# Kernel optimization log

Measured on AMD Instinct MI355X. Metric: run time of the kernel, lower is better.

## Reference

```python
import jax, jax.numpy as jnp
import numpy as np

EPS = 1e-12
SIMILARITY = 'l2'


def setup_inputs() -> dict:
    key = jax.random.key(0)
    k1, k2, k3, k4 = jax.random.split(key, 4)
    N, M, D = 8192, 8192, 256
    x = jax.random.normal(k1, (N, D), dtype=jnp.float32)
    x_n = jax.random.normal(k2, (M, D), dtype=jnp.float32)
    W = jax.random.normal(k3, (D, 2), dtype=jnp.float32) / np.sqrt(D)
    b = jax.random.normal(k4, (2,), dtype=jnp.float32)
    return {"x": x, "x_n": x_n, "W": W, "b": b}


def _sim_matrix(x, x_n, similarity):
    if similarity == 'l2':
        x2 = jnp.sum(x * x, axis=1, keepdims=True)          # [N,1]
        xn2 = jnp.sum(x_n * x_n, axis=1, keepdims=True).T    # [1,M]
        d2 = jnp.maximum(x2 + xn2 - 2.0 * (x @ x_n.T), 0.0)
        return -jnp.sqrt(d2)
    elif similarity == 'l1':
        return -jnp.sum(jnp.abs(x[:, None, :] - x_n[None, :, :]), axis=-1)
    elif similarity == 'dot':
        return (x @ x_n.T) / x.shape[1]
    elif similarity == 'cos':
        xn_ = x / jnp.linalg.norm(x, axis=1, keepdims=True)
        xnn = x_n / jnp.linalg.norm(x_n, axis=1, keepdims=True)
        return xn_ @ xnn.T
    raise ValueError(similarity)


def reference(x, x_n, W, b) -> jnp.ndarray:
    # soft-KNN params from a small linear head
    params = jax.nn.sigmoid(x @ W + b)                      # [N,2]
    k = jnp.clip(params[:, 0:1], EPS, 1.0 - EPS)            # [N,1]
    t = jnp.clip(params[:, 1:2], EPS, 1.0 - EPS)            # [N,1]

    sim = _sim_matrix(x, x_n, SIMILARITY)                   # [N,M]
    sim_min = jnp.min(sim, axis=1, keepdims=True)
    sim_max = jnp.max(sim, axis=1, keepdims=True)
    sim = (sim - sim_min) / (sim_max - sim_min)             # row min-max normalize
    sim = jnp.maximum(sim, EPS)

    shift = t / (1.0 - t) * (k - sim) * jnp.log(sim / k)
    return sim + jnp.where(sim <= k, shift, 0.0)
```

## Files before the change

### kernel.cpp

```cpp
#include <hip/hip_runtime.h>
#include <hip/hip_bf16.h>
#include <cstdint>

#define N_ROWS 8192
#define M_ROWS 8192
#define DDIM   256
#define EPSF   1e-12f

typedef unsigned short u16;
typedef __attribute__((ext_vector_type(8))) short short8;
typedef __attribute__((ext_vector_type(4))) float floatx4;

__device__ inline void split_bf16(float v, u16& h, u16& lo) {
    __hip_bfloat16 hb = __float2bfloat16(v);
    float hf = __bfloat162float(hb);
    __hip_bfloat16 lb = __float2bfloat16(v - hf);
    h  = __builtin_bit_cast(u16, hb);
    lo = __builtin_bit_cast(u16, lb);
}

__global__ __launch_bounds__(256) void prep_x(
    const float* __restrict__ x, const float* __restrict__ W, const float* __restrict__ b,
    u16* __restrict__ xhi, u16* __restrict__ xlo,
    float* __restrict__ x2, float* __restrict__ karr, float* __restrict__ Carr,
    float* __restrict__ logkarr)
{
    const int l = threadIdx.x & 63;
    const int w = threadIdx.x >> 6;
    const int row = blockIdx.x * 4 + w;

    const float4 xv = *(const float4*)(x + (size_t)row * DDIM + l * 4);
    const float4 wa = *(const float4*)(W + l * 8);
    const float4 wb = *(const float4*)(W + l * 8 + 4);

    float s2 = xv.x * xv.x + xv.y * xv.y + xv.z * xv.z + xv.w * xv.w;
    float s0 = xv.x * wa.x + xv.y * wa.z + xv.z * wb.x + xv.w * wb.z;
    float s1 = xv.x * wa.y + xv.y * wa.w + xv.z * wb.y + xv.w * wb.w;

    u16 h0, l0, h1, l1, h2, l2, h3, l3;
    split_bf16(xv.x, h0, l0); split_bf16(xv.y, h1, l1);
    split_bf16(xv.z, h2, l2); split_bf16(xv.w, h3, l3);
    *(ushort4*)(xhi + (size_t)row * DDIM + l * 4) = make_ushort4(h0, h1, h2, h3);
    *(ushort4*)(xlo + (size_t)row * DDIM + l * 4) = make_ushort4(l0, l1, l2, l3);

    #pragma unroll
    for (int off = 32; off; off >>= 1) {
        s2 += __shfl_xor(s2, off);
        s0 += __shfl_xor(s0, off);
        s1 += __shfl_xor(s1, off);
    }
    if (l == 0) {
        float a0 = s0 + b[0];
        float a1 = s1 + b[1];
        float k = 1.0f / (1.0f + __expf(-a0));
        float t = 1.0f / (1.0f + __expf(-a1));
        k = fminf(fmaxf(k, EPSF), 1.0f - EPSF);
        t = fminf(fmaxf(t, EPSF), 1.0f - EPSF);
        x2[row] = s2;
        karr[row] = k;
        Carr[row] = t / (1.0f - t);
        logkarr[row] = logf(k);
    }
}

__global__ __launch_bounds__(256) void prep_xn(
    const float* __restrict__ xn,
    u16* __restrict__ xnhi, u16* __restrict__ xnlo, float* __restrict__ xn2)
{
    const int l = threadIdx.x & 63;
    const int w = threadIdx.x >> 6;
    const int row = blockIdx.x * 4 + w;

    const float4 xv = *(const float4*)(xn + (size_t)row * DDIM + l * 4);
    float s2 = xv.x * xv.x + xv.y * xv.y + xv.z * xv.z + xv.w * xv.w;

    u16 h0, l0, h1, l1, h2, l2, h3, l3;
    split_bf16(xv.x, h0, l0); split_bf16(xv.y, h1, l1);
    split_bf16(xv.z, h2, l2); split_bf16(xv.w, h3, l3);
    *(ushort4*)(xnhi + (size_t)row * DDIM + l * 4) = make_ushort4(h0, h1, h2, h3);
    *(ushort4*)(xnlo + (size_t)row * DDIM + l * 4) = make_ushort4(l0, l1, l2, l3);

    #pragma unroll
    for (int off = 32; off; off >>= 1) s2 += __shfl_xor(s2, off);
    if (l == 0) xn2[row] = s2;
}

__global__ __launch_bounds__(256) void gemm_s(
    const u16* __restrict__ xhi, const u16* __restrict__ xlo,
    const u16* __restrict__ xnhi, const u16* __restrict__ xnlo,
    const float* __restrict__ x2, const float* __restrict__ xn2,
    float* __restrict__ out)
{
    __shared__ u16 lds[16384];

    const int l  = threadIdx.x & 63;
    const int w  = threadIdx.x >> 6;
    const int wm = w >> 1;
    const int wn = w & 1;
    const int bRow = blockIdx.y;
    const int bCol = blockIdx.x;

    floatx4 acc[4][4];
    #pragma unroll
    for (int mi = 0; mi < 4; ++mi)
        #pragma unroll
        for (int ni = 0; ni < 4; ++ni)
            acc[mi][ni] = (floatx4){0.f, 0.f, 0.f, 0.f};

    const u16* bases[4] = {xhi, xlo, xnhi, xnlo};
    const int lrow = l & 15;
    const int lk8  = (l >> 4) * 8;

    for (int kk = 0; kk < DDIM / 32; ++kk) {
        const int ks = kk * 32;
        #pragma unroll
        for (int p = 0; p < 8; ++p) {
            const int id    = w * 8 + p;
            const int panel = id >> 3;
            const int tile  = id & 7;
            const int grow  = (panel < 2 ? bRow : bCol) * 128 + tile * 16 + lrow;
            const u16* src  = bases[panel] + (size_t)grow * DDIM + ks + lk8;
            u16* dst = &lds[panel * 4096 + tile * 512];
            __builtin_amdgcn_global_load_lds(
                (const __attribute__((address_space(1))) void*)src,
                (__attribute__((address_space(3))) void*)dst,
                16, 0, 0);
        }
        __syncthreads();

        short8 ah[4], al[4], bh[4], bl[4];
        #pragma unroll
        for (int i = 0; i < 4; ++i) {
            ah[i] = *(const short8*)&lds[0     + (wm * 4 + i) * 512 + l * 8];
            al[i] = *(const short8*)&lds[4096  + (wm * 4 + i) * 512 + l * 8];
            bh[i] = *(const short8*)&lds[8192  + (wn * 4 + i) * 512 + l * 8];
            bl[i] = *(const short8*)&lds[12288 + (wn * 4 + i) * 512 + l * 8];
        }
        #pragma unroll
        for (int mi = 0; mi < 4; ++mi)
            #pragma unroll
            for (int ni = 0; ni < 4; ++ni) {
                acc[mi][ni] = __builtin_amdgcn_mfma_f32_16x16x32_bf16(ah[mi], bh[ni], acc[mi][ni], 0, 0, 0);
                acc[mi][ni] = __builtin_amdgcn_mfma_f32_16x16x32_bf16(ah[mi], bl[ni], acc[mi][ni], 0, 0, 0);
                acc[mi][ni] = __builtin_amdgcn_mfma_f32_16x16x32_bf16(al[mi], bh[ni], acc[mi][ni], 0, 0, 0);
            }
        __syncthreads();
    }

    const int q  = l >> 4;
    const int cn = l & 15;
    #pragma unroll
    for (int mi = 0; mi < 4; ++mi) {
        #pragma unroll
        for (int r = 0; r < 4; ++r) {
            const int i = bRow * 128 + wm * 64 + mi * 16 + q * 4 + r;
            const float x2i = x2[i];
            #pragma unroll
            for (int ni = 0; ni < 4; ++ni) {
                const int j = bCol * 128 + wn * 64 + ni * 16 + cn;
                const float d2 = x2i + xn2[j] - 2.0f * acc[mi][ni][r];
                out[(size_t)i * M_ROWS + j] = -sqrtf(fmaxf(d2, 0.0f));
            }
        }
    }
}

__global__ __launch_bounds__(256) void transform_row(
    float* __restrict__ out, const float* __restrict__ x, const float* __restrict__ xn,
    const float* __restrict__ karr, const float* __restrict__ Carr,
    const float* __restrict__ logkarr)
{
    const int row = blockIdx.x;
    const int t = threadIdx.x;
    const int l = t & 63;
    const int w = t >> 6;

    __shared__ float wmin[4], wmax[4];
    __shared__ int cnt;
    __shared__ unsigned long long sMinBits;
    __shared__ int cidx[1024];
    __shared__ double cval[1024];

    const size_t rbase = (size_t)row * M_ROWS;
    float4 v[8];
    #pragma unroll
    for (int c = 0; c < 8; ++c)
        v[c] = *(const float4*)(out + rbase + c * 1024 + t * 4);

    float lmin = 1e30f, lmax = -1e30f;
    #pragma unroll
    for (int c = 0; c < 8; ++c) {
        lmin = fminf(lmin, fminf(fminf(v[c].x, v[c].y), fminf(v[c].z, v[c].w)));
        lmax = fmaxf(lmax, fmaxf(fmaxf(v[c].x, v[c].y), fmaxf(v[c].z, v[c].w)));
    }
    #pragma unroll
    for (int m = 1; m < 64; m <<= 1) {
        lmin = fminf(lmin, __shfl_xor(lmin, m));
        lmax = fmaxf(lmax, __shfl_xor(lmax, m));
    }
    if (l == 0) { wmin[w] = lmin; wmax[w] = lmax; }
    if (t == 0) { cnt = 0; sMinBits = 0ull; }
    __syncthreads();
    const float sminA = fminf(fminf(wmin[0], wmin[1]), fminf(wmin[2], wmin[3]));
    const float smaxA = fmaxf(fmaxf(wmax[0], wmax[1]), fmaxf(wmax[2], wmax[3]));
    const float thresh = sminA + 0.05f * (smaxA - sminA);

    int myPos[8], mySlot[8];
    int myCnt = 0;
    #pragma unroll
    for (int c = 0; c < 8; ++c) {
        const float* pv = (const float*)&v[c];
        #pragma unroll
        for (int u = 0; u < 4; ++u) {
            if (pv[u] <= thresh) {
                int pos = atomicAdd(&cnt, 1);
                if (pos < 1024 && myCnt < 8) {
                    cidx[pos] = c * 1024 + t * 4 + u;
                    myPos[myCnt] = pos;
                    mySlot[myCnt] = c * 4 + u;
                    myCnt++;
                }
            }
        }
    }
    __syncthreads();
    const int nc = min(cnt, 1024);

    const float4 xa = *(const float4*)(x + (size_t)row * DDIM + l * 4);
    const double dx0 = xa.x, dx1 = xa.y, dx2 = xa.z, dx3 = xa.w;
    double x2p = dx0 * dx0 + dx1 * dx1 + dx2 * dx2 + dx3 * dx3;
    #pragma unroll
    for (int m = 1; m < 64; m <<= 1) x2p += __shfl_xor(x2p, m);

    for (int c = w; c < nc; c += 4) {
        const int j = cidx[c];
        const float4 na = *(const float4*)(xn + (size_t)j * DDIM + l * 4);
        const double n0 = na.x, n1 = na.y, n2 = na.z, n3 = na.w;
        double dot = dx0 * n0 + dx1 * n1 + dx2 * n2 + dx3 * n3;
        double nn  = n0 * n0 + n1 * n1 + n2 * n2 + n3 * n3;
        #pragma unroll
        for (int m = 1; m < 64; m <<= 1) {
            dot += __shfl_xor(dot, m);
            nn  += __shfl_xor(nn, m);
        }
        if (l == 0) {
            double d2 = x2p + nn - 2.0 * dot;
            d2 = d2 > 0.0 ? d2 : 0.0;
            double se = -sqrt(d2);
            cval[c] = se;
            atomicMax(&sMinBits, (unsigned long long)__double_as_longlong(se));
        }
    }
    __syncthreads();

    const double sminD = __longlong_as_double((long long)sMinBits);
    const float k = karr[row], C = Carr[row], logk = logkarr[row];
    const float smin = (float)sminD;
    const double invD = 1.0 / ((double)smaxA - sminD);
    const float inv = (float)invD;

    float o[32];
    #pragma unroll
    for (int c = 0; c < 8; ++c) {
        const float* pv = (const float*)&v[c];
        #pragma unroll
        for (int u = 0; u < 4; ++u) {
            float sim = fmaxf((pv[u] - smin) * inv, EPSF);
            float r = sim;
            if (sim <= k) r += C * (k - sim) * (__logf(sim) - logk);
            o[c * 4 + u] = r;
        }
    }
    for (int q2 = 0; q2 < myCnt; ++q2) {
        double simd = (cval[myPos[q2]] - sminD) * invD;
        simd = simd > (double)EPSF ? simd : (double)EPSF;
        float sim = (float)simd;
        float r = sim;
        if (sim <= k) r += C * (k - sim) * (logf(sim) - logk);
        o[mySlot[q2]] = r;
    }
    #pragma unroll
    for (int c = 0; c < 8; ++c) {
        float4 ov;
        ov.x = o[c * 4 + 0]; ov.y = o[c * 4 + 1];
        ov.z = o[c * 4 + 2]; ov.w = o[c * 4 + 3];
        *(float4*)(out + rbase + c * 1024 + t * 4) = ov;
    }
}

extern "C" void kernel_launch(void* const* d_in, const int* in_sizes, int n_in,
                              void* d_out, int out_size, void* d_ws, size_t ws_size,
                              hipStream_t stream)
{
    const float* x  = (const float*)d_in[0];
    const float* xn = (const float*)d_in[1];
    const float* W  = (const float*)d_in[2];
    const float* b  = (const float*)d_in[3];
    float* out = (float*)d_out;

    uint8_t* ws = (uint8_t*)d_ws;
    u16* xhi  = (u16*)(ws);
    u16* xlo  = (u16*)(ws + (4u << 20));
    u16* xnhi = (u16*)(ws + (8u << 20));
    u16* xnlo = (u16*)(ws + (12u << 20));
    float* x2       = (float*)(ws + (16u << 20));
    float* xn2      = x2 + N_ROWS;
    float* karr     = xn2 + M_ROWS;
    float* Carr     = karr + N_ROWS;
    float* logkarr  = Carr + N_ROWS;

    prep_x<<<N_ROWS / 4, 256, 0, stream>>>(x, W, b, xhi, xlo, x2, karr, Carr, logkarr);
    prep_xn<<<M_ROWS / 4, 256, 0, stream>>>(xn, xnhi, xnlo, xn2);
    gemm_s<<<dim3(M_ROWS / 128, N_ROWS / 128), 256, 0, stream>>>(
        xhi, xlo, xnhi, xnlo, x2, xn2, out);
    transform_row<<<N_ROWS, 256, 0, stream>>>(out, x, xn, karr, Carr, logkarr);
}
```

Measured before the change: 517.7 us.

## Rewrite split-bf16 GEMM with 256x256 tiles, double-buffered swizzled LDS

Replaces the 128x128 GEMM tile with a 256x256 tile computed by 512 threads, each wave holding an 8x4 grid of MFMA accumulators. The three hi/lo product terms are laid out as 12 K-stages and loaded straight into LDS with double buffering, so global loads overlap with MFMA work. An XOR swizzle avoids LDS bank conflicts, and a grouped block-order swizzle improves L2 reuse. The cost is 128KB of dynamic LDS, which means one block per CU, plus higher register pressure.

```diff
diff --git a/kernel.cpp b/kernel.cpp
--- a/kernel.cpp
+++ b/kernel.cpp
@@ -85,79 +85,110 @@
     if (l == 0) xn2[row] = s2;
 }
 
-__global__ __launch_bounds__(256) void gemm_s(
+__global__ __launch_bounds__(512, 2) void gemm_s(
     const u16* __restrict__ xhi, const u16* __restrict__ xlo,
     const u16* __restrict__ xnhi, const u16* __restrict__ xnlo,
     const float* __restrict__ x2, const float* __restrict__ xn2,
     float* __restrict__ out)
 {
-    __shared__ u16 lds[16384];
-
-    const int l  = threadIdx.x & 63;
-    const int w  = threadIdx.x >> 6;
-    const int wm = w >> 1;
-    const int wn = w & 1;
-    const int bRow = blockIdx.y;
-    const int bCol = blockIdx.x;
-
-    floatx4 acc[4][4];
-    #pragma unroll
-    for (int mi = 0; mi < 4; ++mi)
+    extern __shared__ char lds[];
+
+    const int tid = threadIdx.x;
+    const int l   = tid & 63;
+    const int w   = tid >> 6;
+    const int wm  = w >> 2;
+    const int wn  = w & 3;
+
+    const int wg   = blockIdx.x;
+    const int swz  = (wg & 7) * 128 + (wg >> 3);
+    const int bRow = swz >> 5;
+    const int bCol = swz & 31;
+
+    const int srow = tid >> 3;
+    const int scol = (((tid & 7) ^ ((tid >> 3) & 7)) << 3);
+    const size_t aSrc = (size_t)(bRow * 256 + srow) * DDIM + scol;
+    const size_t bSrc = (size_t)(bCol * 256 + srow) * DDIM + scol;
+
+#define STAGE(T, BUF) do {                                                        \
+    const u16* pa_ = ((T) < 8) ? xhi : xlo;                                       \
+    const u16* pb_ = (((T) >> 2) == 1) ? xnlo : xnhi;                             \
+    const int  ko_ = ((T) & 3) * 64;                                              \
+    char* da_ = lds + (BUF) * 65536;                                              \
+    char* db_ = da_ + 32768;                                                      \
+    _Pragma("unroll")                                                             \
+    for (int j_ = 0; j_ < 4; ++j_) {                                              \
+        __builtin_amdgcn_global_load_lds(                                         \
+            (const __attribute__((address_space(1))) void*)(pa_ + aSrc + (size_t)j_ * 16384 + ko_), \
+            (__attribute__((address_space(3))) void*)(da_ + j_ * 8192 + tid * 16), 16, 0, 0); \
+        __builtin_amdgcn_global_load_lds(                                         \
+            (const __attribute__((address_space(1))) void*)(pb_ + bSrc + (size_t)j_ * 16384 + ko_), \
+            (__attribute__((address_space(3))) void*)(db_ + j_ * 8192 + tid * 16), 16, 0, 0); \
+    } } while (0)
+
+    floatx4 acc[8][4];
+    #pragma unroll
+    for (int mi = 0; mi < 8; ++mi)
         #pragma unroll
         for (int ni = 0; ni < 4; ++ni)
             acc[mi][ni] = (floatx4){0.f, 0.f, 0.f, 0.f};
 
-    const u16* bases[4] = {xhi, xlo, xnhi, xnlo};
-    const int lrow = l & 15;
-    const int lk8  = (l >> 4) * 8;
-
-    for (int kk = 0; kk < DDIM / 32; ++kk) {
-        const int ks = kk * 32;
-        #pragma unroll
-        for (int p = 0; p < 8; ++p) {
-            const int id    = w * 8 + p;
-            const int panel = id >> 3;
-            const int tile  = id & 7;
-            const int grow  = (panel < 2 ? bRow : bCol) * 128 + tile * 16 + lrow;
-            const u16* src  = bases[panel] + (size_t)grow * DDIM + ks + lk8;
-            u16* dst = &lds[panel * 4096 + tile * 512];
-            __builtin_amdgcn_global_load_lds(
-                (const __attribute__((address_space(1))) void*)src,
-                (__attribute__((address_space(3))) void*)dst,
-                16, 0, 0);
-        }
-        __syncthreads();
-
-        short8 ah[4], al[4], bh[4], bl[4];
-        #pragma unroll
-        for (int i = 0; i < 4; ++i) {
-            ah[i] = *(const short8*)&lds[0     + (wm * 4 + i) * 512 + l * 8];
-            al[i] = *(const short8*)&lds[4096  + (wm * 4 + i) * 512 + l * 8];
-            bh[i] = *(const short8*)&lds[8192  + (wn * 4 + i) * 512 + l * 8];
-            bl[i] = *(const short8*)&lds[12288 + (wn * 4 + i) * 512 + l * 8];
-        }
-        #pragma unroll
-        for (int mi = 0; mi < 4; ++mi)
+    const int laneRow = l & 15;
+    const int laneKb  = (l >> 4) << 4;
+    const int laneSwz = (l & 7) << 4;
+    const int aRowB = (wm * 128 + laneRow) * 128;
+    const int bRowB = (wn * 64  + laneRow) * 128;
+
+    STAGE(0, 0);
+    STAGE(1, 1);
+
+    for (int t = 0; t < 12; ++t) {
+        if (t < 11) asm volatile("s_waitcnt vmcnt(8)" ::: "memory");
+        else        asm volatile("s_waitcnt vmcnt(0)" ::: "memory");
+        __builtin_amdgcn_s_barrier();
+
+        const char* pA = lds + (t & 1) * 65536;
+        const char* pB = pA + 32768;
+
+        #pragma unroll
+        for (int ks = 0; ks < 2; ++ks) {
+            const int kb = (ks * 64 + laneKb) ^ laneSwz;
+            short8 ah[8], bh[4];
             #pragma unroll
-            for (int ni = 0; ni < 4; ++ni) {
-                acc[mi][ni] = __builtin_amdgcn_mfma_f32_16x16x32_bf16(ah[mi], bh[ni], acc[mi][ni], 0, 0, 0);
-                acc[mi][ni] = __builtin_amdgcn_mfma_f32_16x16x32_bf16(ah[mi], bl[ni], acc[mi][ni], 0, 0, 0);
-                acc[mi][ni] = __builtin_amdgcn_mfma_f32_16x16x32_bf16(al[mi], bh[ni], acc[mi][ni], 0, 0, 0);
-            }
-        __syncthreads();
-    }
+            for (int mi = 0; mi < 8; ++mi)
+                ah[mi] = *(const short8*)(pA + aRowB + mi * 2048 + kb);
+            #pragma unroll
+            for (int ni = 0; ni < 4; ++ni)
+                bh[ni] = *(const short8*)(pB + bRowB + ni * 2048 + kb);
+            asm volatile("s_waitcnt lgkmcnt(0)" ::: "memory");
+            __builtin_amdgcn_sched_barrier(0);
+            __builtin_amdgcn_s_setprio(1);
+            #pragma unroll
+            for (int mi = 0; mi < 8; ++mi)
+                #pragma unroll
+                for (int ni = 0; ni < 4; ++ni)
+                    acc[mi][ni] = __builtin_amdgcn_mfma_f32_16x16x32_bf16(ah[mi], bh[ni], acc[mi][ni], 0, 0, 0);
+            __builtin_amdgcn_s_setprio(0);
+            __builtin_amdgcn_sched_barrier(0);
+            if (ks == 0) __builtin_amdgcn_s_barrier();
+        }
+        __builtin_amdgcn_s_barrier();
+        if (t + 2 < 12) STAGE(t + 2, t & 1);
+    }
+#undef STAGE
 
     const int q  = l >> 4;
     const int cn = l & 15;
-    #pragma unroll
-    for (int mi = 0; mi < 4; ++mi) {
+    const int rowBase = bRow * 256 + wm * 128;
+    const int colBase = bCol * 256 + wn * 64;
+    #pragma unroll
+    for (int mi = 0; mi < 8; ++mi) {
         #pragma unroll
         for (int r = 0; r < 4; ++r) {
-            const int i = bRow * 128 + wm * 64 + mi * 16 + q * 4 + r;
+            const int i = rowBase + mi * 16 + q * 4 + r;
             const float x2i = x2[i];
             #pragma unroll
             for (int ni = 0; ni < 4; ++ni) {
-                const int j = bCol * 128 + wn * 64 + ni * 16 + cn;
+                const int j = colBase + ni * 16 + cn;
                 const float d2 = x2i + xn2[j] - 2.0f * acc[mi][ni][r];
                 out[(size_t)i * M_ROWS + j] = -sqrtf(fmaxf(d2, 0.0f));
             }
@@ -309,9 +340,15 @@
     float* Carr     = karr + N_ROWS;
     float* logkarr  = Carr + N_ROWS;
 
+    static bool attr_done = false;
+    if (!attr_done) {
+        (void)hipFuncSetAttribute(reinterpret_cast<const void*>(gemm_s),
+                                  hipFuncAttributeMaxDynamicSharedMemorySize, 131072);
+        attr_done = true;
+    }
+
     prep_x<<<N_ROWS / 4, 256, 0, stream>>>(x, W, b, xhi, xlo, x2, karr, Carr, logkarr);
     prep_xn<<<M_ROWS / 4, 256, 0, stream>>>(xn, xnhi, xnlo, xn2);
-    gemm_s<<<dim3(M_ROWS / 128, N_ROWS / 128), 256, 0, stream>>>(
-        xhi, xlo, xnhi, xnlo, x2, xn2, out);
+    gemm_s<<<1024, 512, 131072, stream>>>(xhi, xlo, xnhi, xnlo, x2, xn2, out);
     transform_row<<<N_ROWS, 256, 0, stream>>>(out, x, xn, karr, Carr, logkarr);
 }
```

After: 475.3 us. -8.2%, faster.
